# Kernel optimization log

Measured on AMD Instinct MI355X. Metric: run time of the kernel, lower is better.

The kernel has to match this reference:

```python
import jax, jax.numpy as jnp
import numpy as np

PLACEHOLDER = -1
B, S, V = 128, 8, 32000  # batch, spec tokens per request, vocab
T = B * S


def setup_inputs() -> dict:
    key = jax.random.key(0)
    ks = jax.random.split(key, 8)
    target_logits = jax.random.normal(ks[0], (T, V), dtype=jnp.float32)
    dp = jax.random.uniform(ks[1], (T, V), dtype=jnp.float32)
    draft_probs = dp / jnp.sum(dp, axis=-1, keepdims=True)  # valid prob dist per token
    draft_token_ids = jax.random.randint(ks[2], (T,), 0, V, dtype=jnp.int32)
    bonus_token_ids = jax.random.randint(ks[3], (B,), 0, V, dtype=jnp.int32)
    temperature = 0.5 + jax.random.uniform(ks[4], (B,), dtype=jnp.float32)  # >0 => all random
    uniform_probs = jax.random.uniform(ks[5], (T,), dtype=jnp.float32)
    # q ~ Exponential(1), as torch's q.exponential_()
    u = jax.random.uniform(ks[6], (B, V), dtype=jnp.float32, minval=1e-10, maxval=1.0)
    q = -jnp.log(u)
    cu_num_draft_tokens = (jnp.arange(B, dtype=jnp.int32) + 1) * S
    return {
        'target_logits': target_logits,
        'draft_probs': draft_probs,
        'draft_token_ids': draft_token_ids,
        'bonus_token_ids': bonus_token_ids,
        'temperature': temperature,
        'uniform_probs': uniform_probs,
        'q': q,
        'cu_num_draft_tokens': cu_num_draft_tokens,
    }


def reference(target_logits, draft_probs, draft_token_ids, bonus_token_ids,
              temperature, uniform_probs, q, cu_num_draft_tokens):
    # compute_probs: softmax of logits / per-token expanded temperature
    temp_tok = jnp.repeat(temperature, S)  # [T]
    target_probs = jax.nn.softmax(target_logits / temp_tok[:, None], axis=-1)  # [T, V]

    tok = jnp.arange(T)
    req = tok // S  # request index per token (uniform raggedness)

    # accept/reject: target_prob/draft_prob >= u  (guard draft_prob > 0)
    p_tgt = target_probs[tok, draft_token_ids]  # [T]
    p_drf = draft_probs[tok, draft_token_ids]   # [T]
    accept = (p_drf > 0) & (p_tgt >= uniform_probs * p_drf)  # [T]

    # recovered tokens: argmax(max(p_tgt - p_drf, 0) / q) over vocab (Gumbel-max trick)
    resid = jnp.maximum(target_probs - draft_probs, 0.0)  # [T, V]
    recovered = jnp.argmax(resid / q[req], axis=-1).astype(jnp.int32)  # [T]

    # sequential accept until first rejection, then placeholder; bonus if all accepted
    accept_b = accept.reshape(B, S)
    alive = jnp.concatenate(
        [jnp.ones((B, 1), dtype=bool),
         jnp.cumprod(accept_b[:, :-1].astype(jnp.int32), axis=1).astype(bool)],
        axis=1)  # alive[b, p] = all accepts before pos p
    tok_out = jnp.where(accept_b, draft_token_ids.reshape(B, S), recovered.reshape(B, S))
    main = jnp.where(alive, tok_out, PLACEHOLDER)  # [B, S]
    all_acc = jnp.all(accept_b, axis=1)
    bonus_col = jnp.where(all_acc, bonus_token_ids, PLACEHOLDER)  # [B]
    output_token_ids = jnp.concatenate([main, bonus_col[:, None]], axis=1)  # [B, S+1]
    return output_token_ids
```

## Files before the change

kernel.cpp:

```cpp
#include <hip/hip_runtime.h>


constexpr int PLACEHOLDER = -1;
constexpr int B = 128;
constexpr int S = 8;
constexpr int V = 32000;
constexpr int T = B * S;
constexpr int NV4 = V / 4;

extern "C" __device__ float __builtin_amdgcn_exp2f(float);
extern "C" __device__ float __builtin_amdgcn_rcpf(float);

__global__ __launch_bounds__(512)
void k1_sum(const float* __restrict__ logits,
            const float* __restrict__ dprobs,
            const int*   __restrict__ draft_ids,
            const float* __restrict__ temperature,
            const float* __restrict__ uniform_probs,
            float* __restrict__ w_D,
            int*   __restrict__ w_acc)
{
    const int t   = blockIdx.x;
    const int tid = threadIdx.x, lane = tid & 63, wid = tid >> 6;
    __shared__ float s_red[8];

    const float c = 1.4426950408889634f / temperature[t >> 3];
    const float4* lrow = (const float4*)(logits + (size_t)t * V);

    int dt = 0; float l_d = 0.f, d_d = 0.f, u = 0.f;
    if (tid == 0) {
        dt  = draft_ids[t];
        l_d = logits[(size_t)t * V + dt];
        d_d = dprobs[(size_t)t * V + dt];
        u   = uniform_probs[t];
    }

    float lsum = 0.f;
    #pragma unroll 4
    for (int j = 0; j < 16; ++j) {
        const int i4 = j * 512 + tid;
        if (i4 < NV4) {
            const float4 v = lrow[i4];
            lsum += (__builtin_amdgcn_exp2f(v.x * c) +
                     __builtin_amdgcn_exp2f(v.y * c)) +
                    (__builtin_amdgcn_exp2f(v.z * c) +
                     __builtin_amdgcn_exp2f(v.w * c));
        }
    }
    #pragma unroll
    for (int off = 32; off >= 1; off >>= 1)
        lsum += __shfl_xor(lsum, off, 64);
    if (lane == 0) s_red[wid] = lsum;
    __syncthreads();
    if (tid == 0) {
        const float D = ((s_red[0] + s_red[1]) + (s_red[2] + s_red[3])) +
                        ((s_red[4] + s_red[5]) + (s_red[6] + s_red[7]));
        w_D[t] = D;
        const float e_d = __builtin_amdgcn_exp2f(l_d * c);
        w_acc[t] = (d_d > 0.f) && (e_d >= u * d_d * D);
    }
}

__global__ __launch_bounds__(1024)
void k2_fin(const float* __restrict__ logits,
            const float* __restrict__ dprobs,
            const float* __restrict__ q,
            const int*   __restrict__ draft_ids,
            const int*   __restrict__ bonus_ids,
            const float* __restrict__ temperature,
            const float* __restrict__ w_D,
            const int*   __restrict__ w_acc,
            int* __restrict__ out)
{
    const int b   = blockIdx.x;
    const int tid = threadIdx.x, lane = tid & 63, wid = tid >> 6;
    __shared__ float s_val[16];
    __shared__ int   s_idx[16];
    __shared__ int   s_needp;

    const float c = 1.4426950408889634f / temperature[b];

    if (wid == 0) {
        const int acc = (lane < S) ? w_acc[b * S + lane] : 1;
        const int dt  = (lane < S) ? draft_ids[b * S + lane] : 0;
        const unsigned long long rej = __ballot(lane < S && !acc) & 0xFFull;
        const int need_p = rej ? (int)__builtin_ctzll(rej) : S;
        if (lane < S)
            out[b * (S + 1) + lane] = (lane < need_p) ? dt : PLACEHOLDER;
        if (lane == 0) {
            out[b * (S + 1) + S] = (need_p == S) ? bonus_ids[b] : PLACEHOLDER;
            s_needp = need_p;
        }
    }
    __syncthreads();
    const int need_p = s_needp;
    if (need_p >= S) return;

    const int   t = b * S + need_p;
    const float D = w_D[t];
    const float4* lrow = (const float4*)(logits + (size_t)t * V);
    const float4* drow = (const float4*)(dprobs + (size_t)t * V);
    const float4* qrow = (const float4*)(q      + (size_t)b * V);

    float bestv = -__builtin_inff();
    int   besti = 0x7fffffff;

#define RS_COMP(LC, DC, QC, GIDX)                                          \
    {                                                                      \
        const float e  = __builtin_amdgcn_exp2f((LC) * c);                 \
        const float rq = __builtin_amdgcn_rcpf(QC);                        \
        const float r  = fmaf(-((DC) * rq), D, e * rq);                    \
        if (r > bestv) { bestv = r; besti = (GIDX); }                      \
    }

    #pragma unroll
    for (int ph = 0; ph < 2; ++ph) {
        float4 lv[4], dv[4], qv[4];
        #pragma unroll
        for (int j = 0; j < 4; ++j) {
            const int i4 = (ph * 4 + j) * 1024 + tid;
            if (i4 < NV4) lv[j] = lrow[i4];
        }
        #pragma unroll
        for (int j = 0; j < 4; ++j) {
            const int i4 = (ph * 4 + j) * 1024 + tid;
            if (i4 < NV4) dv[j] = drow[i4];
        }
        #pragma unroll
        for (int j = 0; j < 4; ++j) {
            const int i4 = (ph * 4 + j) * 1024 + tid;
            if (i4 < NV4) qv[j] = qrow[i4];
        }
        #pragma unroll
        for (int j = 0; j < 4; ++j) {
            const int i4 = (ph * 4 + j) * 1024 + tid;
            if (i4 < NV4) {
                const int base = i4 * 4;
                RS_COMP(lv[j].x, dv[j].x, qv[j].x, base + 0)
                RS_COMP(lv[j].y, dv[j].y, qv[j].y, base + 1)
                RS_COMP(lv[j].z, dv[j].z, qv[j].z, base + 2)
                RS_COMP(lv[j].w, dv[j].w, qv[j].w, base + 3)
            }
        }
    }
#undef RS_COMP

    #pragma unroll
    for (int off = 32; off >= 1; off >>= 1) {
        const float ov = __shfl_xor(bestv, off, 64);
        const int   oi = __shfl_xor(besti, off, 64);
        if (ov > bestv || (ov == bestv && oi < besti)) { bestv = ov; besti = oi; }
    }
    if (lane == 0) { s_val[wid] = bestv; s_idx[wid] = besti; }
    __syncthreads();
    if (wid == 0) {
        float bv = (lane < 16) ? s_val[lane] : -__builtin_inff();
        int   bi = (lane < 16) ? s_idx[lane] : 0x7fffffff;
        #pragma unroll
        for (int off = 8; off >= 1; off >>= 1) {
            const float ov = __shfl_xor(bv, off, 64);
            const int   oi = __shfl_xor(bi, off, 64);
            if (ov > bv || (ov == bv && oi < bi)) { bv = ov; bi = oi; }
        }
        if (lane == 0)
            out[b * (S + 1) + need_p] = bi;
    }
}

extern "C" void kernel_launch(void* const* d_in, const int* in_sizes, int n_in,
                              void* d_out, int out_size, void* d_ws, size_t ws_size,
                              hipStream_t stream) {
    const float* logits      = (const float*)d_in[0];
    const float* dprobs      = (const float*)d_in[1];
    const int*   draft_ids   = (const int*)d_in[2];
    const int*   bonus_ids   = (const int*)d_in[3];
    const float* temperature = (const float*)d_in[4];
    const float* uniform     = (const float*)d_in[5];
    const float* q           = (const float*)d_in[6];

    int* out = (int*)d_out;
    float* w_D   = (float*)d_ws;
    int*   w_acc = (int*)(w_D + T);

    k1_sum<<<T, 512, 0, stream>>>(logits, dprobs, draft_ids, temperature,
                                  uniform, w_D, w_acc);
    k2_fin<<<B, 1024, 0, stream>>>(logits, dprobs, q, draft_ids, bonus_ids,
                                   temperature, w_D, w_acc, out);
}
```

Measured before the change: 36.23 us.

## Fuse softmax-sum and recovery into one per-request kernel with early exit

Replaces the two-kernel scheme, where one block per token computed every softmax denominator, with a single kernel of one block per request. Each block walks the draft positions in order, prefetching the next row of logits into registers, and stops at the first rejection. It then reuses the cached logits row for the argmax over residuals. This skips denominator work for positions after a rejection and removes one launch and the workspace round trip. The cost is that only 128 blocks each process up to 8 rows one after another, which lowers parallelism and makes the kernel latency-bound, and the large register arrays may limit occupancy.

Result: faster. 31.79 us (-12.2%).

```diff
diff --git a/kernel.cpp b/kernel.cpp
--- a/kernel.cpp
+++ b/kernel.cpp
@@ -5,100 +5,108 @@
 constexpr int B = 128;
 constexpr int S = 8;
 constexpr int V = 32000;
-constexpr int T = B * S;
 constexpr int NV4 = V / 4;
 
 extern "C" __device__ float __builtin_amdgcn_exp2f(float);
 extern "C" __device__ float __builtin_amdgcn_rcpf(float);
 
-__global__ __launch_bounds__(512)
-void k1_sum(const float* __restrict__ logits,
-            const float* __restrict__ dprobs,
-            const int*   __restrict__ draft_ids,
-            const float* __restrict__ temperature,
-            const float* __restrict__ uniform_probs,
-            float* __restrict__ w_D,
-            int*   __restrict__ w_acc)
-{
-    const int t   = blockIdx.x;
-    const int tid = threadIdx.x, lane = tid & 63, wid = tid >> 6;
-    __shared__ float s_red[8];
-
-    const float c = 1.4426950408889634f / temperature[t >> 3];
-    const float4* lrow = (const float4*)(logits + (size_t)t * V);
-
-    int dt = 0; float l_d = 0.f, d_d = 0.f, u = 0.f;
-    if (tid == 0) {
-        dt  = draft_ids[t];
-        l_d = logits[(size_t)t * V + dt];
-        d_d = dprobs[(size_t)t * V + dt];
-        u   = uniform_probs[t];
-    }
-
-    float lsum = 0.f;
-    #pragma unroll 4
-    for (int j = 0; j < 16; ++j) {
-        const int i4 = j * 512 + tid;
-        if (i4 < NV4) {
-            const float4 v = lrow[i4];
-            lsum += (__builtin_amdgcn_exp2f(v.x * c) +
-                     __builtin_amdgcn_exp2f(v.y * c)) +
-                    (__builtin_amdgcn_exp2f(v.z * c) +
-                     __builtin_amdgcn_exp2f(v.w * c));
-        }
-    }
-    #pragma unroll
-    for (int off = 32; off >= 1; off >>= 1)
-        lsum += __shfl_xor(lsum, off, 64);
-    if (lane == 0) s_red[wid] = lsum;
-    __syncthreads();
-    if (tid == 0) {
-        const float D = ((s_red[0] + s_red[1]) + (s_red[2] + s_red[3])) +
-                        ((s_red[4] + s_red[5]) + (s_red[6] + s_red[7]));
-        w_D[t] = D;
-        const float e_d = __builtin_amdgcn_exp2f(l_d * c);
-        w_acc[t] = (d_d > 0.f) && (e_d >= u * d_d * D);
-    }
-}
-
-__global__ __launch_bounds__(1024)
-void k2_fin(const float* __restrict__ logits,
+__global__ __launch_bounds__(1024, 4)
+void rs_seq(const float* __restrict__ logits,
             const float* __restrict__ dprobs,
             const float* __restrict__ q,
             const int*   __restrict__ draft_ids,
             const int*   __restrict__ bonus_ids,
             const float* __restrict__ temperature,
-            const float* __restrict__ w_D,
-            const int*   __restrict__ w_acc,
+            const float* __restrict__ uniform_probs,
             int* __restrict__ out)
 {
     const int b   = blockIdx.x;
     const int tid = threadIdx.x, lane = tid & 63, wid = tid >> 6;
+    __shared__ float s_red[16];
+    __shared__ float s_ld[S], s_dd[S], s_u[S];
+    __shared__ int   s_dt[S];
+    __shared__ int   s_bonus;
+    __shared__ float s_D;
+    __shared__ int   s_dec;
     __shared__ float s_val[16];
     __shared__ int   s_idx[16];
-    __shared__ int   s_needp;
 
     const float c = 1.4426950408889634f / temperature[b];
 
     if (wid == 0) {
-        const int acc = (lane < S) ? w_acc[b * S + lane] : 1;
-        const int dt  = (lane < S) ? draft_ids[b * S + lane] : 0;
-        const unsigned long long rej = __ballot(lane < S && !acc) & 0xFFull;
-        const int need_p = rej ? (int)__builtin_ctzll(rej) : S;
-        if (lane < S)
-            out[b * (S + 1) + lane] = (lane < need_p) ? dt : PLACEHOLDER;
-        if (lane == 0) {
-            out[b * (S + 1) + S] = (need_p == S) ? bonus_ids[b] : PLACEHOLDER;
-            s_needp = need_p;
+        if (lane < S) {
+            const int t  = b * S + lane;
+            const int dt = draft_ids[t];
+            s_dt[lane] = dt;
+            s_u[lane]  = uniform_probs[t];
+            s_ld[lane] = logits[(size_t)t * V + dt];
+            s_dd[lane] = dprobs[(size_t)t * V + dt];
+        }
+        if (lane == 8) s_bonus = bonus_ids[b];
+    }
+
+    float4 cur[8], nxt[8];
+    {
+        const float4* lrow = (const float4*)(logits + (size_t)(b * S) * V);
+        #pragma unroll
+        for (int j = 0; j < 8; ++j) {
+            const int i4 = j * 1024 + tid;
+            if (i4 < NV4) cur[j] = lrow[i4];
         }
     }
-    __syncthreads();
-    const int need_p = s_needp;
-    if (need_p >= S) return;
+
+    int   need_p = S;
+    float Dsave  = 0.f;
+
+    for (int p = 0; p < S; ++p) {
+        if (p + 1 < S) {
+            const float4* lrn =
+                (const float4*)(logits + (size_t)(b * S + p + 1) * V);
+            #pragma unroll
+            for (int j = 0; j < 8; ++j) {
+                const int i4 = j * 1024 + tid;
+                if (i4 < NV4) nxt[j] = lrn[i4];
+            }
+        }
+        float lsum = 0.f;
+        #pragma unroll
+        for (int j = 0; j < 8; ++j) {
+            const int i4 = j * 1024 + tid;
+            if (i4 < NV4) {
+                const float4 v = cur[j];
+                lsum += (__builtin_amdgcn_exp2f(v.x * c) +
+                         __builtin_amdgcn_exp2f(v.y * c)) +
+                        (__builtin_amdgcn_exp2f(v.z * c) +
+                         __builtin_amdgcn_exp2f(v.w * c));
+            }
+        }
+        #pragma unroll
+        for (int off = 32; off >= 1; off >>= 1)
+            lsum += __shfl_xor(lsum, off, 64);
+        if (lane == 0) s_red[wid] = lsum;
+        __syncthreads();
+        if (tid == 0) {
+            float D = 0.f;
+            #pragma unroll
+            for (int w = 0; w < 16; ++w) D += s_red[w];
+            const float e_d = __builtin_amdgcn_exp2f(s_ld[p] * c);
+            s_dec = (s_dd[p] > 0.f) && (e_d >= s_u[p] * s_dd[p] * D);
+            s_D   = D;
+        }
+        __syncthreads();
+        if (!s_dec) { need_p = p; Dsave = s_D; break; }
+        #pragma unroll
+        for (int j = 0; j < 8; ++j) cur[j] = nxt[j];
+    }
+
+    if (need_p >= S) {
+        if (tid < S) out[b * (S + 1) + tid] = s_dt[tid];
+        if (tid == 0) out[b * (S + 1) + S] = s_bonus;
+        return;
+    }
 
     const int   t = b * S + need_p;
-    const float D = w_D[t];
-    const float4* lrow = (const float4*)(logits + (size_t)t * V);
+    const float D = Dsave;
     const float4* drow = (const float4*)(dprobs + (size_t)t * V);
     const float4* qrow = (const float4*)(q      + (size_t)b * V);
 
@@ -115,12 +123,7 @@
 
     #pragma unroll
     for (int ph = 0; ph < 2; ++ph) {
-        float4 lv[4], dv[4], qv[4];
-        #pragma unroll
-        for (int j = 0; j < 4; ++j) {
-            const int i4 = (ph * 4 + j) * 1024 + tid;
-            if (i4 < NV4) lv[j] = lrow[i4];
-        }
+        float4 dv[4], qv[4];
         #pragma unroll
         for (int j = 0; j < 4; ++j) {
             const int i4 = (ph * 4 + j) * 1024 + tid;
@@ -133,13 +136,15 @@
         }
         #pragma unroll
         for (int j = 0; j < 4; ++j) {
-            const int i4 = (ph * 4 + j) * 1024 + tid;
+            const int jj = ph * 4 + j;
+            const int i4 = jj * 1024 + tid;
             if (i4 < NV4) {
-                const int base = i4 * 4;
-                RS_COMP(lv[j].x, dv[j].x, qv[j].x, base + 0)
-                RS_COMP(lv[j].y, dv[j].y, qv[j].y, base + 1)
-                RS_COMP(lv[j].z, dv[j].z, qv[j].z, base + 2)
-                RS_COMP(lv[j].w, dv[j].w, qv[j].w, base + 3)
+                const float4 lv = cur[jj];
+                const int base  = i4 * 4;
+                RS_COMP(lv.x, dv[j].x, qv[j].x, base + 0)
+                RS_COMP(lv.y, dv[j].y, qv[j].y, base + 1)
+                RS_COMP(lv.z, dv[j].z, qv[j].z, base + 2)
+                RS_COMP(lv.w, dv[j].w, qv[j].w, base + 3)
             }
         }
     }
@@ -162,8 +167,16 @@
             const int   oi = __shfl_xor(bi, off, 64);
             if (ov > bv || (ov == bv && oi < bi)) { bv = ov; bi = oi; }
         }
-        if (lane == 0)
-            out[b * (S + 1) + need_p] = bi;
+        if (lane == 0) {
+            #pragma unroll
+            for (int p = 0; p < S; ++p) {
+                int tok = PLACEHOLDER;
+                if (p < need_p)       tok = s_dt[p];
+                else if (p == need_p) tok = bi;
+                out[b * (S + 1) + p] = tok;
+            }
+            out[b * (S + 1) + S] = PLACEHOLDER;
+        }
     }
 }
 
@@ -179,11 +192,6 @@
     const float* q           = (const float*)d_in[6];
 
     int* out = (int*)d_out;
-    float* w_D   = (float*)d_ws;
-    int*   w_acc = (int*)(w_D + T);
-
-    k1_sum<<<T, 512, 0, stream>>>(logits, dprobs, draft_ids, temperature,
-                                  uniform, w_D, w_acc);
-    k2_fin<<<B, 1024, 0, stream>>>(logits, dprobs, q, draft_ids, bonus_ids,
-                                   temperature, w_D, w_acc, out);
+    rs_seq<<<B, 1024, 0, stream>>>(logits, dprobs, q, draft_ids, bonus_ids,
+                                   temperature, uniform, out);
 }
```
